# Performance work log

Measured on AMD Instinct MI355X. Metric: run time of the kernel, lower is better.

Reference implementation:

```python
import jax, jax.numpy as jnp
import numpy as np

N = 30000
E = 480000
F_IN = 100
HID = 64
HEADS = 4
NCLS = 47
HC = HEADS * HID  # 256
NEG_SLOPE = 0.2
BN_EPS = 1e-5


def setup_inputs() -> dict:
    key = jax.random.key(0)
    ks = jax.random.split(key, 32)
    s = 0.1
    inp = {
        'x': jax.random.normal(ks[0], (N, F_IN), jnp.float32),
        'edge_index': jax.random.randint(ks[1], (2, E), 0, N, jnp.int32),
        # layer 0: GATConv(F_IN -> HID, heads, concat=True)
        'w0': jax.random.normal(ks[2], (F_IN, HC), jnp.float32) * s,
        'as0': jax.random.normal(ks[3], (HEADS, HID), jnp.float32) * s,
        'ad0': jax.random.normal(ks[4], (HEADS, HID), jnp.float32) * s,
        'b0': jnp.zeros((HC,), jnp.float32),
        'sw0': jax.random.normal(ks[5], (F_IN, HC), jnp.float32) * s,
        'sb0': jnp.zeros((HC,), jnp.float32),
        'g0': jnp.ones((HC,), jnp.float32),
        'be0': jnp.zeros((HC,), jnp.float32),
        # layer 1: GATConv(HC -> HID, heads, concat=True)
        'w1': jax.random.normal(ks[6], (HC, HC), jnp.float32) * s,
        'as1': jax.random.normal(ks[7], (HEADS, HID), jnp.float32) * s,
        'ad1': jax.random.normal(ks[8], (HEADS, HID), jnp.float32) * s,
        'b1': jnp.zeros((HC,), jnp.float32),
        'sw1': jax.random.normal(ks[9], (HC, HC), jnp.float32) * s,
        'sb1': jnp.zeros((HC,), jnp.float32),
        'g1': jnp.ones((HC,), jnp.float32),
        'be1': jnp.zeros((HC,), jnp.float32),
        # layer 2: GATConv(HC -> NCLS, heads, concat=False)
        'w2': jax.random.normal(ks[10], (HC, HEADS * NCLS), jnp.float32) * s,
        'as2': jax.random.normal(ks[11], (HEADS, NCLS), jnp.float32) * s,
        'ad2': jax.random.normal(ks[12], (HEADS, NCLS), jnp.float32) * s,
        'b2': jnp.zeros((NCLS,), jnp.float32),
        'sw2': jax.random.normal(ks[13], (HC, NCLS), jnp.float32) * s,
        'sb2': jnp.zeros((NCLS,), jnp.float32),
    }
    return inp


def gat_conv(x, src, dst, W, a_src, a_dst, bias, heads, out_ch, concat):
    # shared linear for src/dst (PyG GATConv with int in_channels)
    h = (x @ W).reshape(N, heads, out_ch)           # [N,H,C]
    al_s = jnp.sum(h * a_src, axis=-1)              # [N,H]
    al_d = jnp.sum(h * a_dst, axis=-1)              # [N,H]
    e = jax.nn.leaky_relu(al_s[src] + al_d[dst], NEG_SLOPE)  # [E,H]
    # segment (per-destination) softmax
    m = jax.ops.segment_max(e, dst, num_segments=N)
    e = jnp.exp(e - m[dst])
    den = jax.ops.segment_sum(e, dst, num_segments=N)
    alpha = e / (den[dst] + 1e-16)                  # [E,H]
    msg = h[src] * alpha[:, :, None]                # [E,H,C]
    out = jax.ops.segment_sum(msg, dst, num_segments=N)  # [N,H,C]
    out = out.reshape(N, heads * out_ch) if concat else out.mean(axis=1)
    return out + bias


def batch_norm(x, gamma, beta):
    mu = jnp.mean(x, axis=0)
    var = jnp.var(x, axis=0)
    return gamma * (x - mu) * jax.lax.rsqrt(var + BN_EPS) + beta


def reference(x, edge_index, w0, as0, ad0, b0, sw0, sb0, g0, be0,
              w1, as1, ad1, b1, sw1, sb1, g1, be1,
              w2, as2, ad2, b2, sw2, sb2):
    src, dst = edge_index[0], edge_index[1]
    # layer 0
    h = gat_conv(x, src, dst, w0, as0, ad0, b0, HEADS, HID, True)
    h = h + x @ sw0 + sb0
    h = jax.nn.elu(batch_norm(h, g0, be0))
    # layer 1
    h2 = gat_conv(h, src, dst, w1, as1, ad1, b1, HEADS, HID, True)
    h2 = h2 + h @ sw1 + sb1
    h2 = jax.nn.elu(batch_norm(h2, g1, be1))
    # layer 2 (concat=False -> mean over heads)
    out = gat_conv(h2, src, dst, w2, as2, ad2, b2, HEADS, NCLS, False)
    out = out + h2 @ sw2 + sb2
    return jax.nn.log_softmax(out, axis=-1)
```

## Files before the change

kernel.cpp:

```cpp
#include <hip/hip_runtime.h>
#include <math.h>

#define NN 30000
#define EE 480000
#define FIN 100
#define NCLS 47
#define SCAN_B 118

typedef unsigned short ushortt;
typedef __attribute__((ext_vector_type(8))) short bf16x8;
typedef __attribute__((ext_vector_type(4))) float f32x4;
typedef __attribute__((ext_vector_type(2))) float f32x2;

__device__ unsigned char g_H8[(size_t)NN * 256];
__device__ ushortt g_Sb[(size_t)NN * 256];
__device__ float   g_S2[(size_t)NN * 48];
__device__ ushortt g_Fb[(size_t)NN * 256];
__device__ ushortt g_Xb[(size_t)NN * 128];
__device__ ushortt g_Wc0[512 * 128];
__device__ ushortt g_Wc1[512 * 256];
__device__ ushortt g_Wc2[235 * 256];
__device__ float g_als[NN * 4];
__device__ float g_ald[NN * 4];
__device__ int   g_rowptr[NN + 1];
__device__ int   g_counts[NN];
__device__ int   g_bsum[128];
__device__ int   g_esrc[EE];
__device__ float g_stat[1024];

__device__ __forceinline__ float wsum(float v) {
#pragma unroll
  for (int o = 32; o > 0; o >>= 1) v += __shfl_xor(v, o, 64);
  return v;
}
__device__ __forceinline__ float lrelu(float x) { return x > 0.f ? x : 0.2f * x; }
__device__ __forceinline__ ushortt f2bf(float f) {
  unsigned int u = __float_as_uint(f);
  unsigned int r = u + 0x7FFF + ((u >> 16) & 1);
  return (ushortt)(r >> 16);
}
__device__ __forceinline__ float bf2f(ushortt u) {
  return __uint_as_float(((unsigned int)u) << 16);
}
__device__ __forceinline__ unsigned int pk4_fp8(float f0, float f1, float f2, float f3) {
  unsigned int r = 0;
  r = __builtin_amdgcn_cvt_pk_fp8_f32(f0, f1, r, false);
  r = __builtin_amdgcn_cvt_pk_fp8_f32(f2, f3, r, true);
  return r;
}
__device__ __forceinline__ int swz(int row, int k) {
  return (k & ~63) | ((((k >> 3) & 7) ^ (row & 7)) << 3) | (k & 7);
}
__device__ __forceinline__ void glds16(const ushortt* gp, ushortt* lp) {
  __builtin_amdgcn_global_load_lds(
      (const __attribute__((address_space(1))) unsigned int*)gp,
      (__attribute__((address_space(3))) unsigned int*)lp, 16, 0, 0);
}

__global__ void count_kernel(const int* __restrict__ dst) {
  int e = blockIdx.x * blockDim.x + threadIdx.x;
  if (e < EE) atomicAdd(&g_counts[dst[e]], 1);
}
__global__ void scan1_kernel() {
  int i = blockIdx.x * 256 + threadIdx.x;
  int v = (i < NN) ? g_counts[i] : 0;
  __shared__ int sh[4];
  float fv = (float)v;
  fv = wsum(fv);
  if ((threadIdx.x & 63) == 0) sh[threadIdx.x >> 6] = (int)fv;
  __syncthreads();
  if (threadIdx.x == 0) g_bsum[blockIdx.x] = sh[0] + sh[1] + sh[2] + sh[3];
}
__global__ void scan2_kernel() {
  __shared__ int sh[128];
  int t = threadIdx.x;
  int v = (t < SCAN_B) ? g_bsum[t] : 0;
  sh[t] = v;
  __syncthreads();
  for (int off = 1; off < 128; off <<= 1) {
    int x = (t >= off) ? sh[t - off] : 0;
    __syncthreads();
    sh[t] += x;
    __syncthreads();
  }
  g_bsum[t] = sh[t] - v;
}
__global__ void scan3_kernel() {
  __shared__ int sh[256];
  int t = threadIdx.x;
  int i = blockIdx.x * 256 + t;
  int v = (i < NN) ? g_counts[i] : 0;
  sh[t] = v;
  __syncthreads();
  for (int off = 1; off < 256; off <<= 1) {
    int x = (t >= off) ? sh[t - off] : 0;
    __syncthreads();
    sh[t] += x;
    __syncthreads();
  }
  if (i < NN) {
    g_rowptr[i] = g_bsum[blockIdx.x] + sh[t] - v;
    g_counts[i] = 0;
  }
  if (i == NN - 1) g_rowptr[NN] = EE;
}
__global__ void scatter_kernel(const int* __restrict__ dst, const int* __restrict__ src) {
  int e = blockIdx.x * blockDim.x + threadIdx.x;
  if (e < EE) {
    int d = dst[e];
    int pos = g_rowptr[d] + atomicAdd(&g_counts[d], 1);
    g_esrc[pos] = src[e];
  }
}

#define CW0 (512 * 128)
#define CW1 (512 * 256)
#define CW2 (235 * 256)
__global__ void conv_kernel(const float* __restrict__ w0, const float* __restrict__ sw0,
                            const float* __restrict__ w1, const float* __restrict__ sw1,
                            const float* __restrict__ w2, const float* __restrict__ sw2,
                            const float* __restrict__ x) {
  int i = blockIdx.x * blockDim.x + threadIdx.x;
  if (i < CW0) {
    int m = i >> 7, k = i & 127;
    float v = 0.f;
    if (k < FIN) v = (m < 256) ? w0[k * 256 + m] : sw0[k * 256 + (m - 256)];
    g_Wc0[(m << 7) | swz(m, k)] = f2bf(v);
    return;
  }
  i -= CW0;
  if (i < CW1) {
    int m = i >> 8, k = i & 255;
    float v = (m < 256) ? w1[k * 256 + m] : sw1[k * 256 + (m - 256)];
    g_Wc1[(m << 8) | swz(m, k)] = f2bf(v);
    return;
  }
  i -= CW1;
  if (i < CW2) {
    int m = i >> 8, k = i & 255;
    float v = (m < 188) ? w2[(size_t)k * 188 + m] : sw2[(size_t)k * 47 + (m - 188)];
    g_Wc2[(m << 8) | swz(m, k)] = f2bf(v);
    return;
  }
  i -= CW2;
  if (i < NN * 128) {
    int r = i >> 7, k = i & 127;
    g_Xb[(r << 7) | swz(r, k)] = (k < FIN) ? f2bf(x[r * FIN + k]) : 0;
    return;
  }
  i -= NN * 128;
  if (i < NN) {
    g_counts[i] = 0;
    return;
  }
  i -= NN;
  if (i < 1024) g_stat[i] = 0.f;
}

__global__ __launch_bounds__(256) void mfma_gemm(
    const ushortt* __restrict__ A, const ushortt* __restrict__ Wt,
    unsigned char* __restrict__ out8, ushortt* __restrict__ out2b,
    float* __restrict__ out2f,
    int nrows, int Kp, int M, int S, int ld8, int ld2,
    const float* __restrict__ bias2, int pad47,
    const float* __restrict__ a_s, const float* __restrict__ a_d,
    float* __restrict__ alsp, float* __restrict__ aldp) {
  __shared__ __align__(16) ushortt smem[12288];
  ushortt* As = smem;
  ushortt* Ws = smem + 64 * 64;
  float* Ls = (float*)smem;
  int t = threadIdx.x;
  int wave = t >> 6, lane = t & 63;
  int row0 = blockIdx.y * 64, col0 = blockIdx.x * 128;
  int wr = wave >> 1, wc = wave & 1;
  int m16 = lane & 15, q = lane >> 4;
  int rin8 = lane >> 3;
  int koff = (lane & 7) * 8;

  f32x4 acc[2][4];
#pragma unroll
  for (int i = 0; i < 2; i++)
#pragma unroll
    for (int j = 0; j < 4; j++) acc[i][j] = (f32x4){0.f, 0.f, 0.f, 0.f};

  for (int k0 = 0; k0 < Kp; k0 += 64) {
#pragma unroll
    for (int r = 0; r < 2; r++) {
      int lrow = wave * 16 + r * 8;
      int ga = min(row0 + lrow + rin8, nrows - 1);
      glds16(A + (size_t)ga * Kp + k0 + koff, &As[lrow * 64]);
    }
#pragma unroll
    for (int r = 0; r < 4; r++) {
      int lrow = wave * 32 + r * 8;
      int gw = min(col0 + lrow + rin8, M - 1);
      glds16(Wt + (size_t)gw * Kp + k0 + koff, &Ws[lrow * 64]);
    }
    __syncthreads();
#pragma unroll
    for (int c = 0; c < 2; c++) {
      bf16x8 af[2], bf[4];
#pragma unroll
      for (int i = 0; i < 2; i++) {
        int row = wr * 32 + i * 16 + m16;
        int ch = (c * 4 + q) ^ (row & 7);
        af[i] = *(const bf16x8*)(&As[row * 64 + ch * 8]);
      }
#pragma unroll
      for (int i = 0; i < 4; i++) {
        int row = wc * 64 + i * 16 + m16;
        int ch = (c * 4 + q) ^ (row & 7);
        bf[i] = *(const bf16x8*)(&Ws[row * 64 + ch * 8]);
      }
#pragma unroll
      for (int rt = 0; rt < 2; rt++)
#pragma unroll
        for (int ct = 0; ct < 4; ct++)
          acc[rt][ct] = __builtin_amdgcn_mfma_f32_16x16x32_bf16(af[rt], bf[ct], acc[rt][ct], 0, 0, 0);
    }
    __syncthreads();
  }

  bool all1 = (!pad47) && (col0 + 128 <= S);
  bool all2 = (col0 >= S);
  int row8 = t >> 3, seg = t & 7;
#pragma unroll
  for (int p = 0; p < 2; p++) {
    __syncthreads();
    if (wr == p) {
#pragma unroll
      for (int rt = 0; rt < 2; rt++) {
#pragma unroll
        for (int ctt = 0; ctt < 4; ctt++) {
#pragma unroll
          for (int reg = 0; reg < 4; reg++) {
            int rloc = rt * 16 + q * 4 + reg;
            Ls[rloc * 132 + wc * 64 + ctt * 16 + m16] = acc[rt][ctt][reg];
          }
        }
      }
    }
    __syncthreads();
    int grow = row0 + p * 32 + row8;
    if (grow < nrows) {
      const float* lrow = Ls + row8 * 132 + seg * 16;
      int cbase = col0 + seg * 16;
      if (all1) {
        unsigned int q8[4];
#pragma unroll
        for (int kk = 0; kk < 4; kk++)
          q8[kk] = pk4_fp8(lrow[kk * 4], lrow[kk * 4 + 1], lrow[kk * 4 + 2], lrow[kk * 4 + 3]);
        uint4 v8 = {q8[0], q8[1], q8[2], q8[3]};
        *(uint4*)(out8 + (size_t)grow * ld8 + cbase) = v8;
        float s_p = 0.f, d_p = 0.f;
#pragma unroll
        for (int kk = 0; kk < 16; kk++) {
          s_p += lrow[kk] * a_s[cbase + kk];
          d_p += lrow[kk] * a_d[cbase + kk];
        }
        s_p += __shfl_xor(s_p, 1, 64); s_p += __shfl_xor(s_p, 2, 64);
        d_p += __shfl_xor(d_p, 1, 64); d_p += __shfl_xor(d_p, 2, 64);
        if ((seg & 3) == 0) {
          int head = cbase >> 6;
          alsp[grow * 4 + head] = s_p;
          aldp[grow * 4 + head] = d_p;
        }
      } else if (all2) {
        const float* brow = bias2 + (cbase - S);
        ushortt* orow = out2b + (size_t)grow * ld2 + (cbase - S);
        unsigned int pk[8];
#pragma unroll
        for (int kk = 0; kk < 8; kk++) {
          unsigned int lo = f2bf(lrow[kk * 2] + brow[kk * 2]);
          unsigned int hi = f2bf(lrow[kk * 2 + 1] + brow[kk * 2 + 1]);
          pk[kk] = lo | (hi << 16);
        }
        uint4 v0 = {pk[0], pk[1], pk[2], pk[3]};
        uint4 v1 = {pk[4], pk[5], pk[6], pk[7]};
        *(uint4*)(orow) = v0;
        *(uint4*)(orow + 8) = v1;
      } else {
        float pa0 = 0.f, pa1 = 0.f, pd0 = 0.f, pd1 = 0.f;
        int h0 = cbase / 47;
        for (int kk = 0; kk < 16; kk++) {
          int c = cbase + kk;
          if (c >= M) break;
          float v = lrow[kk];
          if (c < S) {
            int hd = c / 47, ch = c - hd * 47;
            int c1 = hd * 48 + ch;
            out8[(size_t)grow * ld8 + c1] =
                (unsigned char)(pk4_fp8(v, 0.f, 0.f, 0.f) & 0xFF);
            if (ch == 46) out8[(size_t)grow * ld8 + c1 + 1] = 0;
            float sw = a_s[hd * 47 + ch], dw = a_d[hd * 47 + ch];
            if (hd == h0) { pa0 += v * sw; pd0 += v * dw; }
            else { pa1 += v * sw; pd1 += v * dw; }
          } else {
            out2f[(size_t)grow * ld2 + (c - S)] = v + bias2[c - S];
          }
        }
        if (pad47 && cbase < S) {
          if (pa0 != 0.f || pd0 != 0.f) {
            atomicAdd(&alsp[grow * 4 + h0], pa0);
            atomicAdd(&aldp[grow * 4 + h0], pd0);
          }
          if ((pa1 != 0.f || pd1 != 0.f) && h0 + 1 < 4) {
            atomicAdd(&alsp[grow * 4 + h0 + 1], pa1);
            atomicAdd(&aldp[grow * 4 + h0 + 1], pd1);
          }
        }
      }
    }
  }
}

__global__ __launch_bounds__(64) void attn_kernel(const unsigned char* __restrict__ H8,
                                                  const float* __restrict__ bias,
                                                  ushortt* __restrict__ Sb) {
  __shared__ __align__(16) float p_sh[64 * 4];
  __shared__ int s_sh[64];
  int n = blockIdx.x, lane = threadIdx.x;
  int rs = g_rowptr[n], deg = g_rowptr[n + 1] - rs;
  float4 ald = *(const float4*)(g_ald + n * 4);
  int q = lane >> 4;
  float den0 = 0, den1 = 0, den2 = 0, den3 = 0;
  float a0 = 0, a1 = 0, a2 = 0, a3 = 0;
  for (int base = 0; base < deg; base += 64) {
    int j = base + lane;
    float p0 = 0, p1 = 0, p2 = 0, p3 = 0;
    int s = 0;
    if (j < deg) {
      s = g_esrc[rs + j];
      float4 av = *(const float4*)(g_als + s * 4);
      p0 = __expf(lrelu(av.x + ald.x)); den0 += p0;
      p1 = __expf(lrelu(av.y + ald.y)); den1 += p1;
      p2 = __expf(lrelu(av.z + ald.z)); den2 += p2;
      p3 = __expf(lrelu(av.w + ald.w)); den3 += p3;
    }
    p_sh[lane * 4 + 0] = p0; p_sh[lane * 4 + 1] = p1;
    p_sh[lane * 4 + 2] = p2; p_sh[lane * 4 + 3] = p3;
    s_sh[lane] = s;
    __syncthreads();
    int cnt = min(64, deg - base);
    for (int jj = 0; jj < cnt; jj++) {
      int ss = s_sh[jj];
      float p = p_sh[jj * 4 + q];
      unsigned int hv = *(const unsigned int*)(H8 + (size_t)ss * 256 + 4 * lane);
      f32x2 lo = __builtin_amdgcn_cvt_pk_f32_fp8(hv, false);
      f32x2 hi = __builtin_amdgcn_cvt_pk_f32_fp8(hv, true);
      a0 += p * lo.x;
      a1 += p * lo.y;
      a2 += p * hi.x;
      a3 += p * hi.y;
    }
    __syncthreads();
  }
  den0 = wsum(den0); den1 = wsum(den1); den2 = wsum(den2); den3 = wsum(den3);
  float denq = (q == 0) ? den0 : (q == 1) ? den1 : (q == 2) ? den2 : den3;
  float inv = 1.f / (denq + 1e-16f);
  size_t o = (size_t)n * 256 + 4 * lane;
  ushort4 sv = *(const ushort4*)(Sb + o);
  float4 bv = *(const float4*)(bias + 4 * lane);
  ushort4 ov;
  ov.x = f2bf(a0 * inv + bv.x + bf2f(sv.x));
  ov.y = f2bf(a1 * inv + bv.y + bf2f(sv.y));
  ov.z = f2bf(a2 * inv + bv.z + bf2f(sv.z));
  ov.w = f2bf(a3 * inv + bv.w + bf2f(sv.w));
  *(ushort4*)(Sb + o) = ov;
}

__global__ __launch_bounds__(64) void attn2_kernel(const unsigned char* __restrict__ H8,
                                                   const float* __restrict__ bias,
                                                   const float* __restrict__ S2,
                                                   float* __restrict__ out) {
  __shared__ __align__(16) float p_sh[64 * 4];
  __shared__ int s_sh[64];
  __shared__ float xh[4][48];
  int n = blockIdx.x, lane = threadIdx.x;
  int rs = g_rowptr[n], deg = g_rowptr[n + 1] - rs;
  float4 ald = *(const float4*)(g_ald + n * 4);
  int head = lane / 12;
  float den0 = 0, den1 = 0, den2 = 0, den3 = 0;
  float a0 = 0, a1 = 0, a2 = 0, a3 = 0;
  for (int base = 0; base < deg; base += 64) {
    int j = base + lane;
    float p0 = 0, p1 = 0, p2 = 0, p3 = 0;
    int s = 0;
    if (j < deg) {
      s = g_esrc[rs + j];
      float4 av = *(const float4*)(g_als + s * 4);
      p0 = __expf(lrelu(av.x + ald.x)); den0 += p0;
      p1 = __expf(lrelu(av.y + ald.y)); den1 += p1;
      p2 = __expf(lrelu(av.z + ald.z)); den2 += p2;
      p3 = __expf(lrelu(av.w + ald.w)); den3 += p3;
    }
    p_sh[lane * 4 + 0] = p0; p_sh[lane * 4 + 1] = p1;
    p_sh[lane * 4 + 2] = p2; p_sh[lane * 4 + 3] = p3;
    s_sh[lane] = s;
    __syncthreads();
    int cnt = min(64, deg - base);
    if (lane < 48) {
      for (int jj = 0; jj < cnt; jj++) {
        int ss = s_sh[jj];
        float p = p_sh[jj * 4 + head];
        unsigned int hv = *(const unsigned int*)(H8 + (size_t)ss * 192 + lane * 4);
        f32x2 lo = __builtin_amdgcn_cvt_pk_f32_fp8(hv, false);
        f32x2 hi = __builtin_amdgcn_cvt_pk_f32_fp8(hv, true);
        a0 += p * lo.x;
        a1 += p * lo.y;
        a2 += p * hi.x;
        a3 += p * hi.y;
      }
    }
    __syncthreads();
  }
  den0 = wsum(den0); den1 = wsum(den1); den2 = wsum(den2); den3 = wsum(den3);
  if (lane < 48) {
    float dh = (head == 0) ? den0 : (head == 1) ? den1 : (head == 2) ? den2 : den3;
    float inv = 1.f / (dh + 1e-16f);
    int chin = (lane % 12) * 4;
    xh[head][chin + 0] = a0 * inv;
    xh[head][chin + 1] = a1 * inv;
    xh[head][chin + 2] = a2 * inv;
    xh[head][chin + 3] = a3 * inv;
  }
  __syncthreads();
  float v = 0.f;
  if (lane < NCLS)
    v = 0.25f * (xh[0][lane] + xh[1][lane] + xh[2][lane] + xh[3][lane]) + bias[lane] +
        S2[(size_t)n * NCLS + lane];
  float mv = (lane < NCLS) ? v : -INFINITY;
#pragma unroll
  for (int o = 32; o > 0; o >>= 1) mv = fmaxf(mv, __shfl_xor(mv, o, 64));
  float ex = (lane < NCLS) ? __expf(v - mv) : 0.f;
  float s = wsum(ex);
  if (lane < NCLS) out[(size_t)n * NCLS + lane] = v - mv - logf(s);
}

__global__ void bn_stats_kernel(const ushortt* __restrict__ Sb, float* __restrict__ stat) {
  int c = threadIdx.x;
  int rows = (NN + gridDim.x - 1) / gridDim.x;
  int r0 = blockIdx.x * rows, r1 = min(r0 + rows, NN);
  float s = 0, q = 0;
  for (int r = r0; r < r1; r++) {
    float v = bf2f(Sb[(size_t)r * 256 + c]);
    s += v;
    q += v * v;
  }
  atomicAdd(&stat[c], s);
  atomicAdd(&stat[256 + c], q);
}
__global__ void bn_norm_kernel(const ushortt* __restrict__ Sb, const float* __restrict__ gamma,
                               const float* __restrict__ beta, const float* __restrict__ stat,
                               float* __restrict__ zs, float* __restrict__ zd) {
  int i = blockIdx.x * blockDim.x + threadIdx.x;
  if (i >= NN * 256) return;
  int c = i & 255;
  int r = i >> 8;
  float mu = stat[c] * (1.f / NN);
  float var = stat[256 + c] * (1.f / NN) - mu * mu;
  float v = (bf2f(Sb[i]) - mu) * rsqrtf(var + 1e-5f) * gamma[c] + beta[c];
  v = v > 0.f ? v : (__expf(v) - 1.f);
  g_Fb[(r << 8) | swz(r, c)] = f2bf(v);
  if (zs && i < NN * 4) {
    zs[i] = 0.f;
    zd[i] = 0.f;
  }
}

extern "C" void kernel_launch(void* const* d_in, const int* in_sizes, int n_in,
                              void* d_out, int out_size, void* d_ws, size_t ws_size,
                              hipStream_t stream) {
  const float* x = (const float*)d_in[0];
  const int* ei = (const int*)d_in[1];
  const int* src = ei;
  const int* dst = ei + EE;
  const float* w0 = (const float*)d_in[2];
  const float* as0 = (const float*)d_in[3];
  const float* ad0 = (const float*)d_in[4];
  const float* b0 = (const float*)d_in[5];
  const float* sw0 = (const float*)d_in[6];
  const float* sb0 = (const float*)d_in[7];
  const float* gm0 = (const float*)d_in[8];
  const float* be0 = (const float*)d_in[9];
  const float* w1 = (const float*)d_in[10];
  const float* as1 = (const float*)d_in[11];
  const float* ad1 = (const float*)d_in[12];
  const float* b1 = (const float*)d_in[13];
  const float* sw1 = (const float*)d_in[14];
  const float* sb1 = (const float*)d_in[15];
  const float* gm1 = (const float*)d_in[16];
  const float* be1 = (const float*)d_in[17];
  const float* w2 = (const float*)d_in[18];
  const float* as2 = (const float*)d_in[19];
  const float* ad2 = (const float*)d_in[20];
  const float* b2 = (const float*)d_in[21];
  const float* sw2 = (const float*)d_in[22];
  const float* sb2 = (const float*)d_in[23];
  float* out = (float*)d_out;

  ushortt *Sb, *Fb, *Xb, *Wc0, *Wc1, *Wc2;
  unsigned char* H8;
  float *S2, *als, *ald, *stat;
  hipGetSymbolAddress((void**)&H8, HIP_SYMBOL(g_H8));
  hipGetSymbolAddress((void**)&Sb, HIP_SYMBOL(g_Sb));
  hipGetSymbolAddress((void**)&S2, HIP_SYMBOL(g_S2));
  hipGetSymbolAddress((void**)&Fb, HIP_SYMBOL(g_Fb));
  hipGetSymbolAddress((void**)&Xb, HIP_SYMBOL(g_Xb));
  hipGetSymbolAddress((void**)&Wc0, HIP_SYMBOL(g_Wc0));
  hipGetSymbolAddress((void**)&Wc1, HIP_SYMBOL(g_Wc1));
  hipGetSymbolAddress((void**)&Wc2, HIP_SYMBOL(g_Wc2));
  hipGetSymbolAddress((void**)&als, HIP_SYMBOL(g_als));
  hipGetSymbolAddress((void**)&ald, HIP_SYMBOL(g_ald));
  hipGetSymbolAddress((void**)&stat, HIP_SYMBOL(g_stat));

  conv_kernel<<<(CW0 + CW1 + CW2 + NN * 128 + NN + 1024 + 255) / 256, 256, 0, stream>>>(
      w0, sw0, w1, sw1, w2, sw2, x);

  count_kernel<<<(EE + 255) / 256, 256, 0, stream>>>(dst);
  scan1_kernel<<<SCAN_B, 256, 0, stream>>>();
  scan2_kernel<<<1, 128, 0, stream>>>();
  scan3_kernel<<<SCAN_B, 256, 0, stream>>>();
  scatter_kernel<<<(EE + 255) / 256, 256, 0, stream>>>(dst, src);

  const int gy = (NN + 63) / 64;

  mfma_gemm<<<dim3(4, gy), 256, 0, stream>>>(Xb, Wc0, H8, Sb, nullptr, NN, 128, 512, 256,
                                             256, 256, sb0, 0, as0, ad0, als, ald);
  attn_kernel<<<NN, 64, 0, stream>>>(H8, b0, Sb);
  bn_stats_kernel<<<240, 256, 0, stream>>>(Sb, stat);
  bn_norm_kernel<<<(NN * 256 + 255) / 256, 256, 0, stream>>>(Sb, gm0, be0, stat,
                                                             nullptr, nullptr);

  mfma_gemm<<<dim3(4, gy), 256, 0, stream>>>(Fb, Wc1, H8, Sb, nullptr, NN, 256, 512, 256,
                                             256, 256, sb1, 0, as1, ad1, als, ald);
  attn_kernel<<<NN, 64, 0, stream>>>(H8, b1, Sb);
  bn_stats_kernel<<<240, 256, 0, stream>>>(Sb, stat + 512);
  bn_norm_kernel<<<(NN * 256 + 255) / 256, 256, 0, stream>>>(Sb, gm1, be1, stat + 512,
                                                             als, ald);

  mfma_gemm<<<dim3(2, gy), 256, 0, stream>>>(Fb, Wc2, H8, nullptr, S2, NN, 256, 235, 188,
                                             192, 47, sb2, 1, as2, ad2, als, ald);
  attn2_kernel<<<NN, 64, 0, stream>>>(H8, b2, S2, out);
}
```

Before: 433.4 us.

## Load GEMM operands directly from global into registers with double buffering

Replaces the LDS-staged tile loads (global_load_lds plus barriers) in the MFMA GEMM with direct per-lane 16-byte global loads into registers, software-pipelined across two K sub-steps. This removes LDS traffic and the two __syncthreads per K iteration. In exchange, data shared between waves is no longer shared through LDS, so each wave issues redundant global/L2 loads with less coalescing, and register pressure goes up. It keeps the same swizzled k-chunk permutation, so the dot products stay the same.

```diff
diff --git a/kernel.cpp b/kernel.cpp
--- a/kernel.cpp
+++ b/kernel.cpp
@@ -51,11 +51,6 @@
 __device__ __forceinline__ int swz(int row, int k) {
   return (k & ~63) | ((((k >> 3) & 7) ^ (row & 7)) << 3) | (k & 7);
 }
-__device__ __forceinline__ void glds16(const ushortt* gp, ushortt* lp) {
-  __builtin_amdgcn_global_load_lds(
-      (const __attribute__((address_space(1))) unsigned int*)gp,
-      (__attribute__((address_space(3))) unsigned int*)lp, 16, 0, 0);
-}
 
 __global__ void count_kernel(const int* __restrict__ dst) {
   int e = blockIdx.x * blockDim.x + threadIdx.x;
@@ -165,17 +160,28 @@
     const float* __restrict__ bias2, int pad47,
     const float* __restrict__ a_s, const float* __restrict__ a_d,
     float* __restrict__ alsp, float* __restrict__ aldp) {
-  __shared__ __align__(16) ushortt smem[12288];
-  ushortt* As = smem;
-  ushortt* Ws = smem + 64 * 64;
-  float* Ls = (float*)smem;
+  __shared__ __align__(16) float Ls[32 * 132];
   int t = threadIdx.x;
   int wave = t >> 6, lane = t & 63;
   int row0 = blockIdx.y * 64, col0 = blockIdx.x * 128;
   int wr = wave >> 1, wc = wave & 1;
   int m16 = lane & 15, q = lane >> 4;
-  int rin8 = lane >> 3;
-  int koff = (lane & 7) * 8;
+
+  int rA0 = min(row0 + wr * 32 + m16, nrows - 1);
+  int rA1 = min(row0 + wr * 32 + 16 + m16, nrows - 1);
+  int rB0 = min(col0 + wc * 64 + m16, M - 1);
+  int rB1 = min(col0 + wc * 64 + 16 + m16, M - 1);
+  int rB2 = min(col0 + wc * 64 + 32 + m16, M - 1);
+  int rB3 = min(col0 + wc * 64 + 48 + m16, M - 1);
+  size_t bA0 = (size_t)rA0 * Kp, bA1 = (size_t)rA1 * Kp;
+  size_t bB0 = (size_t)rB0 * Kp, bB1 = (size_t)rB1 * Kp;
+  size_t bB2 = (size_t)rB2 * Kp, bB3 = (size_t)rB3 * Kp;
+  int cA0a = (q ^ (rA0 & 7)) * 8, cA0b = ((4 + q) ^ (rA0 & 7)) * 8;
+  int cA1a = (q ^ (rA1 & 7)) * 8, cA1b = ((4 + q) ^ (rA1 & 7)) * 8;
+  int cB0a = (q ^ (rB0 & 7)) * 8, cB0b = ((4 + q) ^ (rB0 & 7)) * 8;
+  int cB1a = (q ^ (rB1 & 7)) * 8, cB1b = ((4 + q) ^ (rB1 & 7)) * 8;
+  int cB2a = (q ^ (rB2 & 7)) * 8, cB2b = ((4 + q) ^ (rB2 & 7)) * 8;
+  int cB3a = (q ^ (rB3 & 7)) * 8, cB3b = ((4 + q) ^ (rB3 & 7)) * 8;
 
   f32x4 acc[2][4];
 #pragma unroll
@@ -183,42 +189,36 @@
 #pragma unroll
     for (int j = 0; j < 4; j++) acc[i][j] = (f32x4){0.f, 0.f, 0.f, 0.f};
 
-  for (int k0 = 0; k0 < Kp; k0 += 64) {
-#pragma unroll
-    for (int r = 0; r < 2; r++) {
-      int lrow = wave * 16 + r * 8;
-      int ga = min(row0 + lrow + rin8, nrows - 1);
-      glds16(A + (size_t)ga * Kp + k0 + koff, &As[lrow * 64]);
-    }
-#pragma unroll
-    for (int r = 0; r < 4; r++) {
-      int lrow = wave * 32 + r * 8;
-      int gw = min(col0 + lrow + rin8, M - 1);
-      glds16(Wt + (size_t)gw * Kp + k0 + koff, &Ws[lrow * 64]);
-    }
-    __syncthreads();
-#pragma unroll
-    for (int c = 0; c < 2; c++) {
-      bf16x8 af[2], bf[4];
-#pragma unroll
-      for (int i = 0; i < 2; i++) {
-        int row = wr * 32 + i * 16 + m16;
-        int ch = (c * 4 + q) ^ (row & 7);
-        af[i] = *(const bf16x8*)(&As[row * 64 + ch * 8]);
-      }
-#pragma unroll
-      for (int i = 0; i < 4; i++) {
-        int row = wc * 64 + i * 16 + m16;
-        int ch = (c * 4 + q) ^ (row & 7);
-        bf[i] = *(const bf16x8*)(&Ws[row * 64 + ch * 8]);
-      }
-#pragma unroll
-      for (int rt = 0; rt < 2; rt++)
-#pragma unroll
-        for (int ct = 0; ct < 4; ct++)
-          acc[rt][ct] = __builtin_amdgcn_mfma_f32_16x16x32_bf16(af[rt], bf[ct], acc[rt][ct], 0, 0, 0);
-    }
-    __syncthreads();
+  auto LOADP = [&](bf16x8& A0, bf16x8& A1, bf16x8& B0, bf16x8& B1, bf16x8& B2, bf16x8& B3,
+                   int w, int c) {
+    A0 = *(const bf16x8*)(A + bA0 + w + (c ? cA0b : cA0a));
+    A1 = *(const bf16x8*)(A + bA1 + w + (c ? cA1b : cA1a));
+    B0 = *(const bf16x8*)(Wt + bB0 + w + (c ? cB0b : cB0a));
+    B1 = *(const bf16x8*)(Wt + bB1 + w + (c ? cB1b : cB1a));
+    B2 = *(const bf16x8*)(Wt + bB2 + w + (c ? cB2b : cB2a));
+    B3 = *(const bf16x8*)(Wt + bB3 + w + (c ? cB3b : cB3a));
+  };
+  auto MFMAP = [&](bf16x8 A0, bf16x8 A1, bf16x8 B0, bf16x8 B1, bf16x8 B2, bf16x8 B3) {
+    acc[0][0] = __builtin_amdgcn_mfma_f32_16x16x32_bf16(A0, B0, acc[0][0], 0, 0, 0);
+    acc[0][1] = __builtin_amdgcn_mfma_f32_16x16x32_bf16(A0, B1, acc[0][1], 0, 0, 0);
+    acc[0][2] = __builtin_amdgcn_mfma_f32_16x16x32_bf16(A0, B2, acc[0][2], 0, 0, 0);
+    acc[0][3] = __builtin_amdgcn_mfma_f32_16x16x32_bf16(A0, B3, acc[0][3], 0, 0, 0);
+    acc[1][0] = __builtin_amdgcn_mfma_f32_16x16x32_bf16(A1, B0, acc[1][0], 0, 0, 0);
+    acc[1][1] = __builtin_amdgcn_mfma_f32_16x16x32_bf16(A1, B1, acc[1][1], 0, 0, 0);
+    acc[1][2] = __builtin_amdgcn_mfma_f32_16x16x32_bf16(A1, B2, acc[1][2], 0, 0, 0);
+    acc[1][3] = __builtin_amdgcn_mfma_f32_16x16x32_bf16(A1, B3, acc[1][3], 0, 0, 0);
+  };
+
+  bf16x8 xA0, xA1, xB0, xB1, xB2, xB3;
+  bf16x8 yA0, yA1, yB0, yB1, yB2, yB3;
+  int steps = Kp >> 5;
+  LOADP(xA0, xA1, xB0, xB1, xB2, xB3, 0, 0);
+  for (int s = 0; s < steps; s += 2) {
+    int w = (s >> 1) * 64;
+    LOADP(yA0, yA1, yB0, yB1, yB2, yB3, w, 1);
+    MFMAP(xA0, xA1, xB0, xB1, xB2, xB3);
+    if (s + 2 < steps) LOADP(xA0, xA1, xB0, xB1, xB2, xB3, w + 64, 0);
+    MFMAP(yA0, yA1, yB0, yB1, yB2, yB3);
   }
 
   bool all1 = (!pad47) && (col0 + 128 <= S);
```

Result: slower. 466.3 us (+7.6%).

## Merge CSR build and batch-norm passes into cooperative grid-sync kernels

Applied to the files above, without the earlier changes.

Replaces the five-kernel CSR construction (count, three scan passes, scatter) with one cooperative kernel that uses grid.sync between phases. It also fuses the batch-norm statistics and normalisation kernels into one cooperative kernel per layer. The aim is to cut kernel launch overhead and inter-kernel gaps. In exchange, the normalisation pass now runs on a small persistent grid (240 blocks) with grid-stride loops instead of a full-width grid, and grid.sync carries its own cost.

```diff
diff --git a/kernel.cpp b/kernel.cpp
--- a/kernel.cpp
+++ b/kernel.cpp
@@ -1,5 +1,8 @@
 #include <hip/hip_runtime.h>
+#include <hip/hip_cooperative_groups.h>
 #include <math.h>
+
+namespace cg = cooperative_groups;
 
 #define NN 30000
 #define EE 480000
@@ -24,7 +27,7 @@
 __device__ float g_ald[NN * 4];
 __device__ int   g_rowptr[NN + 1];
 __device__ int   g_counts[NN];
-__device__ int   g_bsum[128];
+__device__ int   g_bsum[256];
 __device__ int   g_esrc[EE];
 __device__ float g_stat[1024];
 
@@ -55,62 +58,6 @@
   __builtin_amdgcn_global_load_lds(
       (const __attribute__((address_space(1))) unsigned int*)gp,
       (__attribute__((address_space(3))) unsigned int*)lp, 16, 0, 0);
-}
-
-__global__ void count_kernel(const int* __restrict__ dst) {
-  int e = blockIdx.x * blockDim.x + threadIdx.x;
-  if (e < EE) atomicAdd(&g_counts[dst[e]], 1);
-}
-__global__ void scan1_kernel() {
-  int i = blockIdx.x * 256 + threadIdx.x;
-  int v = (i < NN) ? g_counts[i] : 0;
-  __shared__ int sh[4];
-  float fv = (float)v;
-  fv = wsum(fv);
-  if ((threadIdx.x & 63) == 0) sh[threadIdx.x >> 6] = (int)fv;
-  __syncthreads();
-  if (threadIdx.x == 0) g_bsum[blockIdx.x] = sh[0] + sh[1] + sh[2] + sh[3];
-}
-__global__ void scan2_kernel() {
-  __shared__ int sh[128];
-  int t = threadIdx.x;
-  int v = (t < SCAN_B) ? g_bsum[t] : 0;
-  sh[t] = v;
-  __syncthreads();
-  for (int off = 1; off < 128; off <<= 1) {
-    int x = (t >= off) ? sh[t - off] : 0;
-    __syncthreads();
-    sh[t] += x;
-    __syncthreads();
-  }
-  g_bsum[t] = sh[t] - v;
-}
-__global__ void scan3_kernel() {
-  __shared__ int sh[256];
-  int t = threadIdx.x;
-  int i = blockIdx.x * 256 + t;
-  int v = (i < NN) ? g_counts[i] : 0;
-  sh[t] = v;
-  __syncthreads();
-  for (int off = 1; off < 256; off <<= 1) {
-    int x = (t >= off) ? sh[t - off] : 0;
-    __syncthreads();
-    sh[t] += x;
-    __syncthreads();
-  }
-  if (i < NN) {
-    g_rowptr[i] = g_bsum[blockIdx.x] + sh[t] - v;
-    g_counts[i] = 0;
-  }
-  if (i == NN - 1) g_rowptr[NN] = EE;
-}
-__global__ void scatter_kernel(const int* __restrict__ dst, const int* __restrict__ src) {
-  int e = blockIdx.x * blockDim.x + threadIdx.x;
-  if (e < EE) {
-    int d = dst[e];
-    int pos = g_rowptr[d] + atomicAdd(&g_counts[d], 1);
-    g_esrc[pos] = src[e];
-  }
 }
 
 #define CW0 (512 * 128)
@@ -155,6 +102,55 @@
   }
   i -= NN;
   if (i < 1024) g_stat[i] = 0.f;
+}
+
+__global__ void csr_coop(const int* __restrict__ dst, const int* __restrict__ src) {
+  cg::grid_group grid = cg::this_grid();
+  int tid = blockIdx.x * blockDim.x + threadIdx.x;
+  int nth = gridDim.x * blockDim.x;
+  for (int e = tid; e < EE; e += nth) atomicAdd(&g_counts[dst[e]], 1);
+  grid.sync();
+  __shared__ int sh[256];
+  int t = threadIdx.x;
+  if (blockIdx.x < SCAN_B) {
+    int i = blockIdx.x * 256 + t;
+    int v = (i < NN) ? g_counts[i] : 0;
+    sh[t] = v;
+    __syncthreads();
+    for (int off = 1; off < 256; off <<= 1) {
+      int xv = (t >= off) ? sh[t - off] : 0;
+      __syncthreads();
+      sh[t] += xv;
+      __syncthreads();
+    }
+    if (i < NN) {
+      g_rowptr[i] = sh[t] - v;
+      g_counts[i] = 0;
+    }
+    if (t == 255) g_bsum[blockIdx.x] = sh[255];
+  }
+  grid.sync();
+  if (blockIdx.x == 0) {
+    int v = (t < SCAN_B) ? g_bsum[t] : 0;
+    sh[t] = v;
+    __syncthreads();
+    for (int off = 1; off < 256; off <<= 1) {
+      int xv = (t >= off) ? sh[t - off] : 0;
+      __syncthreads();
+      sh[t] += xv;
+      __syncthreads();
+    }
+    g_bsum[t] = sh[t] - v;
+  }
+  grid.sync();
+  for (int i = tid; i < NN; i += nth) g_rowptr[i] += g_bsum[i >> 8];
+  if (tid == 0) g_rowptr[NN] = EE;
+  grid.sync();
+  for (int e = tid; e < EE; e += nth) {
+    int d = dst[e];
+    int pos = g_rowptr[d] + atomicAdd(&g_counts[d], 1);
+    g_esrc[pos] = src[e];
+  }
 }
 
 __global__ __launch_bounds__(256) void mfma_gemm(
@@ -437,34 +433,36 @@
   if (lane < NCLS) out[(size_t)n * NCLS + lane] = v - mv - logf(s);
 }
 
-__global__ void bn_stats_kernel(const ushortt* __restrict__ Sb, float* __restrict__ stat) {
+__global__ void bn_coop(const ushortt* __restrict__ Sb, const float* __restrict__ gamma,
+                        const float* __restrict__ beta, float* __restrict__ stat,
+                        float* __restrict__ zs, float* __restrict__ zd) {
+  cg::grid_group grid = cg::this_grid();
   int c = threadIdx.x;
   int rows = (NN + gridDim.x - 1) / gridDim.x;
   int r0 = blockIdx.x * rows, r1 = min(r0 + rows, NN);
-  float s = 0, q = 0;
+  float s = 0, qq = 0;
   for (int r = r0; r < r1; r++) {
     float v = bf2f(Sb[(size_t)r * 256 + c]);
     s += v;
-    q += v * v;
+    qq += v * v;
   }
   atomicAdd(&stat[c], s);
-  atomicAdd(&stat[256 + c], q);
-}
-__global__ void bn_norm_kernel(const ushortt* __restrict__ Sb, const float* __restrict__ gamma,
-                               const float* __restrict__ beta, const float* __restrict__ stat,
-                               float* __restrict__ zs, float* __restrict__ zd) {
-  int i = blockIdx.x * blockDim.x + threadIdx.x;
-  if (i >= NN * 256) return;
-  int c = i & 255;
-  int r = i >> 8;
-  float mu = stat[c] * (1.f / NN);
-  float var = stat[256 + c] * (1.f / NN) - mu * mu;
-  float v = (bf2f(Sb[i]) - mu) * rsqrtf(var + 1e-5f) * gamma[c] + beta[c];
-  v = v > 0.f ? v : (__expf(v) - 1.f);
-  g_Fb[(r << 8) | swz(r, c)] = f2bf(v);
-  if (zs && i < NN * 4) {
-    zs[i] = 0.f;
-    zd[i] = 0.f;
+  atomicAdd(&stat[256 + c], qq);
+  grid.sync();
+  int tid = blockIdx.x * blockDim.x + threadIdx.x;
+  int nth = gridDim.x * blockDim.x;
+  for (int i = tid; i < NN * 256; i += nth) {
+    int cc = i & 255;
+    int r = i >> 8;
+    float mu = stat[cc] * (1.f / NN);
+    float var = stat[256 + cc] * (1.f / NN) - mu * mu;
+    float v = (bf2f(Sb[i]) - mu) * rsqrtf(var + 1e-5f) * gamma[cc] + beta[cc];
+    v = v > 0.f ? v : (__expf(v) - 1.f);
+    g_Fb[(r << 8) | swz(r, cc)] = f2bf(v);
+    if (zs && i < NN * 4) {
+      zs[i] = 0.f;
+      zd[i] = 0.f;
+    }
   }
 }
 
@@ -517,27 +515,36 @@
   conv_kernel<<<(CW0 + CW1 + CW2 + NN * 128 + NN + 1024 + 255) / 256, 256, 0, stream>>>(
       w0, sw0, w1, sw1, w2, sw2, x);
 
-  count_kernel<<<(EE + 255) / 256, 256, 0, stream>>>(dst);
-  scan1_kernel<<<SCAN_B, 256, 0, stream>>>();
-  scan2_kernel<<<1, 128, 0, stream>>>();
-  scan3_kernel<<<SCAN_B, 256, 0, stream>>>();
-  scatter_kernel<<<(EE + 255) / 256, 256, 0, stream>>>(dst, src);
+  {
+    void* args[] = {(void*)&dst, (void*)&src};
+    hipLaunchCooperativeKernel((const void*)csr_coop, dim3(512), dim3(256), args, 0,
+                               stream);
+  }
 
   const int gy = (NN + 63) / 64;
+  float* znull = nullptr;
+  float* stat0 = stat;
+  float* stat1 = stat + 512;
 
   mfma_gemm<<<dim3(4, gy), 256, 0, stream>>>(Xb, Wc0, H8, Sb, nullptr, NN, 128, 512, 256,
                                              256, 256, sb0, 0, as0, ad0, als, ald);
   attn_kernel<<<NN, 64, 0, stream>>>(H8, b0, Sb);
-  bn_stats_kernel<<<240, 256, 0, stream>>>(Sb, stat);
-  bn_norm_kernel<<<(NN * 256 + 255) / 256, 256, 0, stream>>>(Sb, gm0, be0, stat,
-                                                             nullptr, nullptr);
+  {
+    void* args[] = {(void*)&Sb, (void*)&gm0, (void*)&be0, (void*)&stat0,
+                    (void*)&znull, (void*)&znull};
+    hipLaunchCooperativeKernel((const void*)bn_coop, dim3(240), dim3(256), args, 0,
+                               stream);
+  }
 
   mfma_gemm<<<dim3(4, gy), 256, 0, stream>>>(Fb, Wc1, H8, Sb, nullptr, NN, 256, 512, 256,
                                              256, 256, sb1, 0, as1, ad1, als, ald);
   attn_kernel<<<NN, 64, 0, stream>>>(H8, b1, Sb);
-  bn_stats_kernel<<<240, 256, 0, stream>>>(Sb, stat + 512);
-  bn_norm_kernel<<<(NN * 256 + 255) / 256, 256, 0, stream>>>(Sb, gm1, be1, stat + 512,
-                                                             als, ald);
+  {
+    void* args[] = {(void*)&Sb, (void*)&gm1, (void*)&be1, (void*)&stat1,
+                    (void*)&als, (void*)&ald};
+    hipLaunchCooperativeKernel((const void*)bn_coop, dim3(240), dim3(256), args, 0,
+                               stream);
+  }
 
   mfma_gemm<<<dim3(2, gy), 256, 0, stream>>>(Fb, Wc2, H8, nullptr, S2, NN, 256, 235, 188,
                                              192, 47, sb2, 1, as2, ad2, als, ald);
```

New measurement: 831.6 us. 1.92x slower.
